# Kernel optimization log

Hardware: AMD Instinct MI355X
Metric: run time of the kernel (lower is better)

The kernel has to match this reference:

```python
import jax, jax.numpy as jnp
import numpy as np

D_IN = 768
D_OUT = 768
NUM_HEADS = 12
HEAD_DIM = D_OUT // NUM_HEADS


def setup_inputs() -> dict:
    key = jax.random.key(0)
    ks = jax.random.split(key, 6)
    s = 1.0 / np.sqrt(D_IN)
    X = jax.random.normal(ks[0], (4, 2048, D_IN), dtype=jnp.float32)
    Wq = jax.random.uniform(ks[1], (D_IN, D_OUT), jnp.float32, -s, s)
    Wk = jax.random.uniform(ks[2], (D_IN, D_OUT), jnp.float32, -s, s)
    Wv = jax.random.uniform(ks[3], (D_IN, D_OUT), jnp.float32, -s, s)
    Wo = jax.random.uniform(ks[4], (D_OUT, D_OUT), jnp.float32, -s, s)
    bo = jax.random.uniform(ks[5], (D_OUT,), jnp.float32, -s, s)
    return {"X": X, "Wq": Wq, "Wk": Wk, "Wv": Wv, "Wo": Wo, "bo": bo}


def reference(X, Wq, Wk, Wv, Wo, bo):
    b, n, _ = X.shape
    # QKV projections, split heads -> [b, h, n, d]
    def split(t):
        return t.reshape(b, n, NUM_HEADS, HEAD_DIM).transpose(0, 2, 1, 3)
    q = split(X @ Wq)
    k = split(X @ Wk)
    v = split(X @ Wv)
    scores = jnp.einsum('bhqd,bhkd->bhqk', q, k) / np.sqrt(HEAD_DIM).astype(np.float32)
    causal = jnp.triu(jnp.ones((n, n), dtype=bool), k=1)
    scores = jnp.where(causal, -jnp.inf, scores)
    attn = jax.nn.softmax(scores, axis=-1)  # dropout p=0 -> identity
    ctx = jnp.einsum('bhqk,bhkd->bhqd', attn, v)
    ctx = ctx.transpose(0, 2, 1, 3).reshape(b, n, D_OUT)
    return ctx @ Wo + bo
```

## Files before the change

### kernel.cpp

```cpp
#include <hip/hip_runtime.h>
#include <stdint.h>

#define B_  4
#define N_  2048
#define D_  768
#define H_  12
#define HD_ 64
#define M_  (B_*N_)

typedef short bf8 __attribute__((ext_vector_type(8)));
typedef float f32x4 __attribute__((ext_vector_type(4)));

static __device__ __forceinline__ unsigned short f2bf(float f) {
    unsigned u = __float_as_uint(f);
    unsigned r = u + 0x7fffu + ((u >> 16) & 1u);
    return (unsigned short)(r >> 16);
}

static __device__ __forceinline__ unsigned pk2bf(float f0, float f1) {
    return ((__float_as_uint(f1) + 0x8000u) & 0xFFFF0000u) |
           ((__float_as_uint(f0) + 0x8000u) >> 16);
}

#if __has_builtin(__builtin_amdgcn_exp2f)
#define EXP2(x) __builtin_amdgcn_exp2f(x)
#else
#define EXP2(x) exp2f(x)
#endif

#define GLOAD_LDS16(gptr, lptr)                                                   \
    __builtin_amdgcn_global_load_lds(                                             \
        (const __attribute__((address_space(1))) void*)(gptr),                    \
        (__attribute__((address_space(3))) void*)(lptr), 16, 0, 0)

#define QSCALE 0.1803368801111204f

__global__ __launch_bounds__(256) void convert_x(const float* __restrict__ X,
                                                 unsigned short* __restrict__ Xb) {
    const size_t i = ((size_t)blockIdx.x * 256 + threadIdx.x) * 8;
    const float4 a = *(const float4*)(X + i);
    const float4 b = *(const float4*)(X + i + 4);
    ushort4 lo, hi;
    lo.x = f2bf(a.x); lo.y = f2bf(a.y); lo.z = f2bf(a.z); lo.w = f2bf(a.w);
    hi.x = f2bf(b.x); hi.y = f2bf(b.y); hi.z = f2bf(b.z); hi.w = f2bf(b.w);
    *(ushort4*)(Xb + i)     = lo;
    *(ushort4*)(Xb + i + 4) = hi;
}

__global__ __launch_bounds__(256) void transpose_w(
    const float* __restrict__ Wq, const float* __restrict__ Wk,
    const float* __restrict__ Wv, const float* __restrict__ Wo,
    unsigned short* __restrict__ Wqt, unsigned short* __restrict__ Wkt,
    unsigned short* __restrict__ Wvt, unsigned short* __restrict__ Wot)
{
    __shared__ float tile[32][33];
    const int z = blockIdx.z;
    const float* W = (z == 0) ? Wq : (z == 1) ? Wk : (z == 2) ? Wv : Wo;
    unsigned short* Wt = (z == 0) ? Wqt : (z == 1) ? Wkt : (z == 2) ? Wvt : Wot;
    const int k0 = blockIdx.x * 32, n0 = blockIdx.y * 32;
    const int tx = threadIdx.x & 31, ty = threadIdx.x >> 5;
    #pragma unroll
    for (int i = 0; i < 4; ++i)
        tile[ty + 8 * i][tx] = W[(size_t)(k0 + ty + 8 * i) * D_ + n0 + tx];
    __syncthreads();
    #pragma unroll
    for (int i = 0; i < 4; ++i)
        Wt[(size_t)(n0 + ty + 8 * i) * D_ + k0 + tx] = f2bf(tile[tx][ty + 8 * i]);
}

__global__ __launch_bounds__(256) void qkv_mfma(
    const unsigned short* __restrict__ Xb,
    const unsigned short* __restrict__ Wqt, const unsigned short* __restrict__ Wkt,
    const unsigned short* __restrict__ Wvt,
    unsigned short* __restrict__ Qb, unsigned short* __restrict__ Kb,
    unsigned short* __restrict__ Vt)
{
    __shared__ unsigned short As[2][8192];
    __shared__ unsigned short Bs[2][8192];

    const int t = threadIdx.x;
    const int wave = t >> 6, lane = t & 63;
    const int col = lane & 15, quad = lane >> 4;
    const int wm = (wave & 1) * 64, wn = (wave >> 1) * 64;

    const int orig = blockIdx.x;
    const int wgid = (orig & 7) * 144 + (orig >> 3);
    const int m0  = (wgid / 18) * 128;
    const int nm  = wgid % 18;
    const int mat = nm / 6;
    const int n0  = (nm % 6) * 128;
    const unsigned short* Wt = (mat == 0) ? Wqt : (mat == 1) ? Wkt : Wvt;
    const bool sw = (mat != 2);

    const unsigned short* Ag = Xb + (size_t)(m0 + (t >> 2)) * D_ + (t & 3) * 8;
    const unsigned short* Bg = Wt + (size_t)(n0 + (t >> 2)) * D_ + (t & 3) * 8;
    unsigned short* AsD = &As[0][0] + t * 8;
    unsigned short* BsD = &Bs[0][0] + t * 8;

#define QKV_STAGE(bsel, kk)                                                        \
    do {                                                                           \
        GLOAD_LDS16(Ag + (kk),                        AsD + (bsel) * 8192);        \
        GLOAD_LDS16(Ag + (kk) + 32,                   AsD + (bsel) * 8192 + 4096); \
        GLOAD_LDS16(Ag + (size_t)64 * D_ + (kk),      AsD + (bsel) * 8192 + 2048); \
        GLOAD_LDS16(Ag + (size_t)64 * D_ + (kk) + 32, AsD + (bsel) * 8192 + 6144); \
        GLOAD_LDS16(Bg + (kk),                        BsD + (bsel) * 8192);        \
        GLOAD_LDS16(Bg + (kk) + 32,                   BsD + (bsel) * 8192 + 4096); \
        GLOAD_LDS16(Bg + (size_t)64 * D_ + (kk),      BsD + (bsel) * 8192 + 2048); \
        GLOAD_LDS16(Bg + (size_t)64 * D_ + (kk) + 32, BsD + (bsel) * 8192 + 6144); \
    } while (0)

    f32x4 acc[4][4] = {};

    QKV_STAGE(0, 0);
    asm volatile("s_waitcnt vmcnt(0)" ::: "memory");
    __builtin_amdgcn_s_barrier();
    __builtin_amdgcn_sched_barrier(0);

    #pragma unroll 2
    for (int it = 0; it < 12; ++it) {
        const int cur = it & 1;
        if (it + 1 < 12) QKV_STAGE(cur ^ 1, (it + 1) * 64);

        const unsigned short* Ab = &As[cur][0];
        const unsigned short* Bb = &Bs[cur][0];
        #pragma unroll
        for (int ks = 0; ks < 2; ++ks) {
            bf8 a[4], b[4];
            #pragma unroll
            for (int i = 0; i < 4; ++i)
                a[i] = *(const bf8*)(Ab + ks * 4096 + (wm + i * 16 + col) * 32 + quad * 8);
            #pragma unroll
            for (int j = 0; j < 4; ++j)
                b[j] = *(const bf8*)(Bb + ks * 4096 + (wn + j * 16 + col) * 32 + quad * 8);
            if (sw) {
                #pragma unroll
                for (int i = 0; i < 4; ++i)
                    #pragma unroll
                    for (int j = 0; j < 4; ++j)
                        acc[i][j] = __builtin_amdgcn_mfma_f32_16x16x32_bf16(b[j], a[i], acc[i][j], 0, 0, 0);
            } else {
                #pragma unroll
                for (int i = 0; i < 4; ++i)
                    #pragma unroll
                    for (int j = 0; j < 4; ++j)
                        acc[i][j] = __builtin_amdgcn_mfma_f32_16x16x32_bf16(a[i], b[j], acc[i][j], 0, 0, 0);
            }
        }

        asm volatile("s_waitcnt vmcnt(0)" ::: "memory");
        __builtin_amdgcn_s_barrier();
        __builtin_amdgcn_sched_barrier(0);
    }
#undef QKV_STAGE

    if (sw) {
        unsigned short* Out = (mat == 0) ? Qb : Kb;
        const float qsc = (mat == 0) ? QSCALE : 1.0f;
        #pragma unroll
        for (int i = 0; i < 4; ++i) {
            const int token = m0 + wm + i * 16 + col;
            const int bb = token >> 11, nn = token & (N_ - 1);
            #pragma unroll
            for (int j = 0; j < 4; ++j) {
                const int n = n0 + wn + j * 16 + quad * 4;
                const int h = n >> 6, d = n & 63;
                ushort4 pk;
                pk.x = f2bf(acc[i][j][0] * qsc);
                pk.y = f2bf(acc[i][j][1] * qsc);
                pk.z = f2bf(acc[i][j][2] * qsc);
                pk.w = f2bf(acc[i][j][3] * qsc);
                *(ushort4*)(Out + ((size_t)(bb * H_ + h) * N_ + nn) * HD_ + d) = pk;
            }
        }
    } else {
        #pragma unroll
        for (int j = 0; j < 4; ++j) {
            const int n = n0 + wn + j * 16 + col;
            const int h = n >> 6, d = n & 63;
            #pragma unroll
            for (int i = 0; i < 4; ++i) {
                const int mb = m0 + wm + i * 16 + quad * 4;
                const int bb = mb >> 11;
                const int nn = mb & (N_ - 1);
                const int nnp = (nn & ~31) | ((quad >> 1) << 4) | ((quad & 1) << 3) |
                                ((i & 1) << 2);
                ushort4 pk;
                pk.x = f2bf(acc[i][j][0]); pk.y = f2bf(acc[i][j][1]);
                pk.z = f2bf(acc[i][j][2]); pk.w = f2bf(acc[i][j][3]);
                *(ushort4*)(Vt + ((size_t)(bb * H_ + h) * HD_ + d) * N_ + nnp) = pk;
            }
        }
    }
}

#define PS 72

static __device__ __forceinline__ void qk_mfma8(
    const bf8 (&ka)[4][2], bf8 qb0, bf8 qb1, f32x4 (&s)[4])
{
    __builtin_amdgcn_s_setprio(1);
    #pragma unroll
    for (int kc = 0; kc < 4; ++kc) {
        s[kc] = __builtin_amdgcn_mfma_f32_16x16x32_bf16(ka[kc][0], qb0, s[kc], 0, 0, 0);
        s[kc] = __builtin_amdgcn_mfma_f32_16x16x32_bf16(ka[kc][1], qb1, s[kc], 0, 0, 0);
    }
    __builtin_amdgcn_s_setprio(0);
}

static __device__ __forceinline__ void softmax_pack(
    const f32x4 (&s)[4], int k0, int q, bool mask, float& lpart,
    bf8& pb0, bf8& pb1, int quad)
{
    float p[4][4];
    if (mask) {
        #pragma unroll
        for (int kc = 0; kc < 4; ++kc)
            #pragma unroll
            for (int r = 0; r < 4; ++r) {
                const int key = k0 + kc * 16 + quad * 4 + r;
                p[kc][r] = EXP2((key > q) ? -INFINITY : s[kc][r]);
            }
    } else {
        #pragma unroll
        for (int kc = 0; kc < 4; ++kc)
            #pragma unroll
            for (int r = 0; r < 4; ++r) p[kc][r] = EXP2(s[kc][r]);
    }

    #pragma unroll
    for (int kc = 0; kc < 4; ++kc)
        #pragma unroll
        for (int r = 0; r < 4; ++r) lpart += p[kc][r];

    uint4 u0, u1;
    u0.x = pk2bf(p[0][0], p[0][1]); u0.y = pk2bf(p[0][2], p[0][3]);
    u0.z = pk2bf(p[1][0], p[1][1]); u0.w = pk2bf(p[1][2], p[1][3]);
    u1.x = pk2bf(p[2][0], p[2][1]); u1.y = pk2bf(p[2][2], p[2][3]);
    u1.z = pk2bf(p[3][0], p[3][1]); u1.w = pk2bf(p[3][2], p[3][3]);
    pb0 = *(bf8*)&u0;
    pb1 = *(bf8*)&u1;
}

static __device__ __forceinline__ void pv_acc(
    bf8 pb0, bf8 pb1, const bf8 (&va)[4][2], f32x4 (&o)[4])
{
    __builtin_amdgcn_s_setprio(1);
    #pragma unroll
    for (int dc = 0; dc < 4; ++dc) {
        o[dc] = __builtin_amdgcn_mfma_f32_16x16x32_bf16(va[dc][0], pb0, o[dc], 0, 0, 0);
        o[dc] = __builtin_amdgcn_mfma_f32_16x16x32_bf16(va[dc][1], pb1, o[dc], 0, 0, 0);
    }
    __builtin_amdgcn_s_setprio(0);
}

__global__ __launch_bounds__(256, 3) void attn_mfma(
    const unsigned short* __restrict__ Qb,
    const unsigned short* __restrict__ Kb,
    const unsigned short* __restrict__ Vt,
    unsigned short* __restrict__ Ctxb)
{
    __shared__ unsigned short Kl[2][64 * PS];
    __shared__ unsigned short Vl[2][64 * PS];

    const int t = threadIdx.x;
    const int wave = t >> 6;
    const int lane = t & 63;
    const int col  = lane & 15;
    const int quad = lane >> 4;

    const int orig = blockIdx.x;
    const int bid  = (orig & 7) * 96 + (orig >> 3);
    const int bh  = bid >> 4;
    const int x   = bid & 15;
    const int tl  = x, th = 31 - x;
    const int q0L = tl * 64 + wave * 16;
    const int q0H = th * 64 + wave * 16;
    const int qL  = q0L + col;
    const int qH  = q0H + col;

    const unsigned short* Kp = Kb + (size_t)bh * N_ * HD_;
    const unsigned short* Vp = Vt + (size_t)bh * HD_ * N_;
    const unsigned short* QpL = Qb + ((size_t)bh * N_ + q0L) * HD_;
    const unsigned short* QpH = Qb + ((size_t)bh * N_ + q0H) * HD_;

    const bf8 qbL0 = *(const bf8*)(QpL + (size_t)col * HD_ + quad * 8);
    const bf8 qbL1 = *(const bf8*)(QpL + (size_t)col * HD_ + 32 + quad * 8);
    const bf8 qbH0 = *(const bf8*)(QpH + (size_t)col * HD_ + quad * 8);
    const bf8 qbH1 = *(const bf8*)(QpH + (size_t)col * HD_ + 32 + quad * 8);

    f32x4 oL[4] = {}, oH[4] = {};
    float lL = 0.f, lH = 0.f;

    const int srow = t >> 3;
    const int scol = (t & 7) * 8;
    const unsigned short* Kg = Kp + (size_t)srow * HD_ + scol;
    const unsigned short* Vg = Vp + (size_t)srow * N_ + scol;
    const int kO0 = srow * PS + scol;
    const int kO1 = (srow + 32) * PS + scol;

    const int iters = 32 - x;

    uint4 kr0 = *(const uint4*)(Kg);
    uint4 kr1 = *(const uint4*)(Kg + (size_t)32 * HD_);
    uint4 vr0 = *(const uint4*)(Vg);
    uint4 vr1 = *(const uint4*)(Vg + (size_t)32 * N_);
    *(uint4*)(Kl[0] + kO0) = kr0;
    *(uint4*)(Kl[0] + kO1) = kr1;
    *(uint4*)(Vl[0] + kO0) = vr0;
    *(uint4*)(Vl[0] + kO1) = vr1;
    kr0 = *(const uint4*)(Kg + (size_t)64 * HD_);
    kr1 = *(const uint4*)(Kg + (size_t)96 * HD_);
    vr0 = *(const uint4*)(Vg + 64);
    vr1 = *(const uint4*)(Vg + (size_t)32 * N_ + 64);

    for (int kt = 0; kt < iters; ++kt) {
        const int k0 = kt * 64;
        const bool actL = (kt <= tl);
        const unsigned short* Kc = Kl[kt & 1];
        const unsigned short* Vc = Vl[kt & 1];
        unsigned short* Kn = Kl[(kt + 1) & 1];
        unsigned short* Vn = Vl[(kt + 1) & 1];

        __syncthreads();

        if (kt + 1 < iters) {
            *(uint4*)(Kn + kO0) = kr0;
            *(uint4*)(Kn + kO1) = kr1;
            *(uint4*)(Vn + kO0) = vr0;
            *(uint4*)(Vn + kO1) = vr1;
        }
        if (kt + 2 < iters) {
            const size_t k2 = (size_t)(kt + 2) * 64;
            kr0 = *(const uint4*)(Kg + k2 * HD_);
            kr1 = *(const uint4*)(Kg + (k2 + 32) * HD_);
            vr0 = *(const uint4*)(Vg + k2);
            vr1 = *(const uint4*)(Vg + (size_t)32 * N_ + k2);
        }

        bf8 ka[4][2];
        #pragma unroll
        for (int kc = 0; kc < 4; ++kc) {
            ka[kc][0] = *(const bf8*)(Kc + (kc * 16 + col) * PS + quad * 8);
            ka[kc][1] = *(const bf8*)(Kc + (kc * 16 + col) * PS + 32 + quad * 8);
        }

        bf8 va[4][2];
        #pragma unroll
        for (int dc = 0; dc < 4; ++dc) {
            va[dc][0] = *(const bf8*)(Vc + (dc * 16 + col) * PS + quad * 8);
            va[dc][1] = *(const bf8*)(Vc + (dc * 16 + col) * PS + 32 + quad * 8);
        }

        f32x4 sH[4] = {};
        qk_mfma8(ka, qbH0, qbH1, sH);
        f32x4 sL[4] = {};
        if (actL) qk_mfma8(ka, qbL0, qbL1, sL);

        bf8 pbH0, pbH1;
        softmax_pack(sH, k0, qH, kt == th, lH, pbH0, pbH1, quad);
        pv_acc(pbH0, pbH1, va, oH);

        if (actL) {
            bf8 pbL0, pbL1;
            softmax_pack(sL, k0, qL, kt == tl, lL, pbL0, pbL1, quad);
            pv_acc(pbL0, pbL1, va, oL);
        }
    }

    const int b = bh / H_;
    const int h = bh % H_;
    {
        float l = lH;
        l += __shfl_xor(l, 16, 64);
        l += __shfl_xor(l, 32, 64);
        const float inv = 1.0f / l;
        unsigned short* cp = Ctxb + ((size_t)(b * N_ + qH)) * D_ + h * HD_;
        #pragma unroll
        for (int dc = 0; dc < 4; ++dc) {
            uint2 pk;
            pk.x = pk2bf(oH[dc][0] * inv, oH[dc][1] * inv);
            pk.y = pk2bf(oH[dc][2] * inv, oH[dc][3] * inv);
            *(uint2*)(cp + dc * 16 + quad * 4) = pk;
        }
    }
    {
        float l = lL;
        l += __shfl_xor(l, 16, 64);
        l += __shfl_xor(l, 32, 64);
        const float inv = 1.0f / l;
        unsigned short* cp = Ctxb + ((size_t)(b * N_ + qL)) * D_ + h * HD_;
        #pragma unroll
        for (int dc = 0; dc < 4; ++dc) {
            uint2 pk;
            pk.x = pk2bf(oL[dc][0] * inv, oL[dc][1] * inv);
            pk.y = pk2bf(oL[dc][2] * inv, oL[dc][3] * inv);
            *(uint2*)(cp + dc * 16 + quad * 4) = pk;
        }
    }
}

__global__ __launch_bounds__(256) void out_mfma(
    const unsigned short* __restrict__ Ctxb,
    const unsigned short* __restrict__ Wot,
    const float* __restrict__ bo,
    float* __restrict__ Out)
{
    __shared__ unsigned short As[2][8192];
    __shared__ unsigned short Bs[2][8192];

    const int t = threadIdx.x;
    const int wave = t >> 6, lane = t & 63;
    const int col = lane & 15, quad = lane >> 4;
    const int wm = (wave & 1) * 64, wn = (wave >> 1) * 64;

    const int orig = blockIdx.x;
    const int wgid = (orig & 7) * 48 + (orig >> 3);
    const int m0 = (wgid / 6) * 128;
    const int n0 = (wgid % 6) * 128;

    const unsigned short* Ag = Ctxb + (size_t)(m0 + (t >> 2)) * D_ + (t & 3) * 8;
    const unsigned short* Bg = Wot + (size_t)(n0 + (t >> 2)) * D_ + (t & 3) * 8;
    unsigned short* AsD = &As[0][0] + t * 8;
    unsigned short* BsD = &Bs[0][0] + t * 8;

#define OUT_STAGE(bsel, kk)                                                        \
    do {                                                                           \
        GLOAD_LDS16(Ag + (kk),                        AsD + (bsel) * 8192);        \
        GLOAD_LDS16(Ag + (kk) + 32,                   AsD + (bsel) * 8192 + 4096); \
        GLOAD_LDS16(Ag + (size_t)64 * D_ + (kk),      AsD + (bsel) * 8192 + 2048); \
        GLOAD_LDS16(Ag + (size_t)64 * D_ + (kk) + 32, AsD + (bsel) * 8192 + 6144); \
        GLOAD_LDS16(Bg + (kk),                        BsD + (bsel) * 8192);        \
        GLOAD_LDS16(Bg + (kk) + 32,                   BsD + (bsel) * 8192 + 4096); \
        GLOAD_LDS16(Bg + (size_t)64 * D_ + (kk),      BsD + (bsel) * 8192 + 2048); \
        GLOAD_LDS16(Bg + (size_t)64 * D_ + (kk) + 32, BsD + (bsel) * 8192 + 6144); \
    } while (0)

    f32x4 acc[4][4] = {};

    OUT_STAGE(0, 0);
    asm volatile("s_waitcnt vmcnt(0)" ::: "memory");
    __builtin_amdgcn_s_barrier();
    __builtin_amdgcn_sched_barrier(0);

    #pragma unroll 2
    for (int it = 0; it < 12; ++it) {
        const int cur = it & 1;
        if (it + 1 < 12) OUT_STAGE(cur ^ 1, (it + 1) * 64);

        const unsigned short* Ab = &As[cur][0];
        const unsigned short* Bb = &Bs[cur][0];
        #pragma unroll
        for (int ks = 0; ks < 2; ++ks) {
            bf8 a[4], b[4];
            #pragma unroll
            for (int i = 0; i < 4; ++i)
                a[i] = *(const bf8*)(Ab + ks * 4096 + (wm + i * 16 + col) * 32 + quad * 8);
            #pragma unroll
            for (int j = 0; j < 4; ++j)
                b[j] = *(const bf8*)(Bb + ks * 4096 + (wn + j * 16 + col) * 32 + quad * 8);
            #pragma unroll
            for (int i = 0; i < 4; ++i)
                #pragma unroll
                for (int j = 0; j < 4; ++j)
                    acc[i][j] = __builtin_amdgcn_mfma_f32_16x16x32_bf16(b[j], a[i], acc[i][j], 0, 0, 0);
        }

        asm volatile("s_waitcnt vmcnt(0)" ::: "memory");
        __builtin_amdgcn_s_barrier();
        __builtin_amdgcn_sched_barrier(0);
    }
#undef OUT_STAGE

    #pragma unroll
    for (int i = 0; i < 4; ++i) {
        const int m = m0 + wm + i * 16 + col;
        #pragma unroll
        for (int j = 0; j < 4; ++j) {
            const int n = n0 + wn + j * 16 + quad * 4;
            const float4 bias = *(const float4*)(bo + n);
            float4 o;
            o.x = acc[i][j][0] + bias.x;
            o.y = acc[i][j][1] + bias.y;
            o.z = acc[i][j][2] + bias.z;
            o.w = acc[i][j][3] + bias.w;
            *(float4*)(Out + (size_t)m * D_ + n) = o;
        }
    }
}

extern "C" void kernel_launch(void* const* d_in, const int* in_sizes, int n_in,
                              void* d_out, int out_size, void* d_ws, size_t ws_size,
                              hipStream_t stream) {
    const float* X  = (const float*)d_in[0];
    const float* Wq = (const float*)d_in[1];
    const float* Wk = (const float*)d_in[2];
    const float* Wv = (const float*)d_in[3];
    const float* Wo = (const float*)d_in[4];
    const float* bo = (const float*)d_in[5];
    float* out = (float*)d_out;

    const size_t elems = (size_t)M_ * D_;
    const size_t welems = (size_t)D_ * D_;
    unsigned short* Xb  = (unsigned short*)d_ws;
    unsigned short* Wqt = Xb + elems;
    unsigned short* Wkt = Wqt + welems;
    unsigned short* Wvt = Wkt + welems;
    unsigned short* Wot = Wvt + welems;
    unsigned short* Qb  = Wot + welems;
    unsigned short* Kb  = Qb + elems;
    unsigned short* Vt  = Kb + elems;
    unsigned short* Ctxb = Xb;

    convert_x<<<dim3(elems / 2048), 256, 0, stream>>>(X, Xb);
    transpose_w<<<dim3(24, 24, 4), 256, 0, stream>>>(Wq, Wk, Wv, Wo, Wqt, Wkt, Wvt, Wot);

    qkv_mfma<<<dim3(1152), 256, 0, stream>>>(Xb, Wqt, Wkt, Wvt, Qb, Kb, Vt);

    attn_mfma<<<dim3(B_ * H_ * 16), 256, 0, stream>>>(Qb, Kb, Vt, Ctxb);

    out_mfma<<<dim3(384), 256, 0, stream>>>(Ctxb, Wot, bo, out);
}
```

Baseline: 203.4 us.

## Load K/V MFMA fragments directly from global memory instead of LDS staging

Removes the shared-memory double buffer and register prefetch for K and V tiles in the attention kernel. Each wave now reads its MFMA operand fragments directly from global memory every key tile. This eliminates the block barrier and LDS traffic, and frees LDS for higher occupancy. In exchange, the four waves redundantly fetch the same K/V data through the cache, and global load latency is no longer hidden by prefetching.

New measurement: 325.6 us. 1.6x slower.

```diff
diff --git a/kernel.cpp b/kernel.cpp
--- a/kernel.cpp
+++ b/kernel.cpp
@@ -193,8 +193,6 @@
     }
 }
 
-#define PS 72
-
 static __device__ __forceinline__ void qk_mfma8(
     const bf8 (&ka)[4][2], bf8 qb0, bf8 qb1, f32x4 (&s)[4])
 {
@@ -259,9 +257,6 @@
     const unsigned short* __restrict__ Vt,
     unsigned short* __restrict__ Ctxb)
 {
-    __shared__ unsigned short Kl[2][64 * PS];
-    __shared__ unsigned short Vl[2][64 * PS];
-
     const int t = threadIdx.x;
     const int wave = t >> 6;
     const int lane = t & 63;
@@ -291,64 +286,28 @@
     f32x4 oL[4] = {}, oH[4] = {};
     float lL = 0.f, lH = 0.f;
 
-    const int srow = t >> 3;
-    const int scol = (t & 7) * 8;
-    const unsigned short* Kg = Kp + (size_t)srow * HD_ + scol;
-    const unsigned short* Vg = Vp + (size_t)srow * N_ + scol;
-    const int kO0 = srow * PS + scol;
-    const int kO1 = (srow + 32) * PS + scol;
+    const unsigned short* Kf = Kp + (size_t)col * HD_ + quad * 8;
+    const unsigned short* Vf = Vp + (size_t)col * N_ + quad * 8;
 
     const int iters = 32 - x;
-
-    uint4 kr0 = *(const uint4*)(Kg);
-    uint4 kr1 = *(const uint4*)(Kg + (size_t)32 * HD_);
-    uint4 vr0 = *(const uint4*)(Vg);
-    uint4 vr1 = *(const uint4*)(Vg + (size_t)32 * N_);
-    *(uint4*)(Kl[0] + kO0) = kr0;
-    *(uint4*)(Kl[0] + kO1) = kr1;
-    *(uint4*)(Vl[0] + kO0) = vr0;
-    *(uint4*)(Vl[0] + kO1) = vr1;
-    kr0 = *(const uint4*)(Kg + (size_t)64 * HD_);
-    kr1 = *(const uint4*)(Kg + (size_t)96 * HD_);
-    vr0 = *(const uint4*)(Vg + 64);
-    vr1 = *(const uint4*)(Vg + (size_t)32 * N_ + 64);
 
     for (int kt = 0; kt < iters; ++kt) {
         const int k0 = kt * 64;
         const bool actL = (kt <= tl);
-        const unsigned short* Kc = Kl[kt & 1];
-        const unsigned short* Vc = Vl[kt & 1];
-        unsigned short* Kn = Kl[(kt + 1) & 1];
-        unsigned short* Vn = Vl[(kt + 1) & 1];
-
-        __syncthreads();
-
-        if (kt + 1 < iters) {
-            *(uint4*)(Kn + kO0) = kr0;
-            *(uint4*)(Kn + kO1) = kr1;
-            *(uint4*)(Vn + kO0) = vr0;
-            *(uint4*)(Vn + kO1) = vr1;
-        }
-        if (kt + 2 < iters) {
-            const size_t k2 = (size_t)(kt + 2) * 64;
-            kr0 = *(const uint4*)(Kg + k2 * HD_);
-            kr1 = *(const uint4*)(Kg + (k2 + 32) * HD_);
-            vr0 = *(const uint4*)(Vg + k2);
-            vr1 = *(const uint4*)(Vg + (size_t)32 * N_ + k2);
-        }
 
         bf8 ka[4][2];
         #pragma unroll
         for (int kc = 0; kc < 4; ++kc) {
-            ka[kc][0] = *(const bf8*)(Kc + (kc * 16 + col) * PS + quad * 8);
-            ka[kc][1] = *(const bf8*)(Kc + (kc * 16 + col) * PS + 32 + quad * 8);
-        }
-
+            const unsigned short* kr = Kf + (size_t)(k0 + kc * 16) * HD_;
+            ka[kc][0] = *(const bf8*)(kr);
+            ka[kc][1] = *(const bf8*)(kr + 32);
+        }
         bf8 va[4][2];
         #pragma unroll
         for (int dc = 0; dc < 4; ++dc) {
-            va[dc][0] = *(const bf8*)(Vc + (dc * 16 + col) * PS + quad * 8);
-            va[dc][1] = *(const bf8*)(Vc + (dc * 16 + col) * PS + 32 + quad * 8);
+            const unsigned short* vr = Vf + (size_t)(dc * 16) * N_ + k0;
+            va[dc][0] = *(const bf8*)(vr);
+            va[dc][1] = *(const bf8*)(vr + 32);
         }
 
         f32x4 sH[4] = {};
```
